# Optimization experiments

Measured on AMD Instinct MI355X. Metric: run time of the kernel, lower is better.

## Reference

```python
import jax, jax.numpy as jnp
import numpy as np
from jax import lax

B, S, H, E, K = 2, 1024, 2048, 16, 4
CAP = int(B * S * 1.5 * K / E)  # capacity = 768
ALPHA = 0.7

def _mlp2(x, w1, b1, w2, b2):
    return jnp.maximum(x @ w1 + b1, 0.0) @ w2 + b2

def setup_inputs() -> dict:
    key = jax.random.key(0)
    ks = iter(jax.random.split(key, 32))
    def w(shape, scale=0.02):
        return (jax.random.normal(next(ks), shape, dtype=jnp.float32) * scale)
    inp = {
        'hidden_states': jax.random.normal(next(ks), (B, S, H), dtype=jnp.float32),
        'mod_image': jax.random.normal(next(ks), (B, S, H), dtype=jnp.float32),
        'mod_genomic': jax.random.normal(next(ks), (B, S, H), dtype=jnp.float32),
        'g_w1': w((H, H)), 'g_b1': jnp.zeros((H,), jnp.float32),
        'g_w2': w((H, E)), 'g_b2': jnp.zeros((E,), jnp.float32),
        'm_w1': w((H, H)), 'm_b1': jnp.zeros((H,), jnp.float32),
        'm_w2': w((H, H)), 'm_b2': jnp.zeros((H,), jnp.float32),
    }
    for p in ('si', 'sg', 'sc', 'sb'):
        inp[p + '_w1'] = w((H, H // 2)); inp[p + '_b1'] = jnp.zeros((H // 2,), jnp.float32)
        inp[p + '_w2'] = w((H // 2, E)); inp[p + '_b2'] = jnp.zeros((E,), jnp.float32)
    return inp

def reference(hidden_states, mod_image, mod_genomic,
              g_w1, g_b1, g_w2, g_b2,
              si_w1, si_b1, si_w2, si_b2,
              sg_w1, sg_b1, sg_w2, sg_b2,
              sc_w1, sc_b1, sc_w2, sc_b2,
              sb_w1, sb_b1, sb_w2, sb_b2,
              m_w1, m_b1, m_w2, m_b2):
    # generalized router probs over experts
    g_probs = jax.nn.softmax(_mlp2(hidden_states, g_w1, g_b1, g_w2, g_b2), axis=-1)
    # missing-modality representation (clinical + biospecimen are missing)
    miss = _mlp2(hidden_states, m_w1, m_b1, m_w2, m_b2)
    # specialized routers: image, genomic (available) + clinical, biospecimen (use miss)
    s_probs = (jax.nn.softmax(_mlp2(mod_image, si_w1, si_b1, si_w2, si_b2), axis=-1)
               + jax.nn.softmax(_mlp2(mod_genomic, sg_w1, sg_b1, sg_w2, sg_b2), axis=-1)
               + jax.nn.softmax(_mlp2(miss, sc_w1, sc_b1, sc_w2, sc_b2), axis=-1)
               + jax.nn.softmax(_mlp2(miss, sb_w1, sb_b1, sb_w2, sb_b2), axis=-1))
    s_probs = s_probs / 2.0  # divided by len(available_modalities) == 2, as in source
    router_probs = ALPHA * g_probs + (1.0 - ALPHA) * s_probs  # [B,S,E]
    top_k_probs, top_k_idx = lax.top_k(router_probs, K)  # [B,S,K]
    top_k_probs = top_k_probs / top_k_probs.sum(axis=-1, keepdims=True)
    onehot = jax.nn.one_hot(top_k_idx, E, dtype=router_probs.dtype)  # [B,S,K,E]
    dmask = onehot.sum(axis=-2)                               # [B,S,E] (0/1: experts distinct)
    cmask = (onehot * top_k_probs[..., None]).sum(axis=-2)    # [B,S,E]
    dispatch = jnp.zeros((B, S, E, CAP), router_probs.dtype).at[..., 0].set(dmask)
    combine = jnp.zeros((B, S, E, CAP), router_probs.dtype).at[..., 0].set(cmask)
    mean_probs = router_probs.mean(axis=(0, 1))  # [E]
    aux_loss = jnp.sum(mean_probs * jnp.log(mean_probs * E + 1e-9))
    return dispatch, combine, router_probs, aux_loss
```

## Files before the change

### kernel.cpp

```cpp
#include <hip/hip_runtime.h>
#include <math.h>
#include <stdint.h>

#define NTOK 2048
#define HDIM 2048
#define HHALF 1024
#define EDIM 16
#define CAPV 768
#define TOPK 4
#define GK 2048

typedef __bf16 bf16x8 __attribute__((ext_vector_type(8)));
typedef __bf16 bf16x4 __attribute__((ext_vector_type(4)));
typedef float f32x4 __attribute__((ext_vector_type(4)));


struct GJobA {
  const __bf16 *Ah, *Al, *Wh, *Wl;
  const float* bias;
  float* Cf; __bf16 *Ch, *Cl;
  int relu, N, blk0;
};
struct GJobsA { GJobA j[6]; };

#define BKA 32
#define NTA 64

#define BARR __builtin_amdgcn_s_barrier()
#define SCHED0 __builtin_amdgcn_sched_barrier(0)
#define PRIO1 __builtin_amdgcn_s_setprio(1)
#define PRIO0 __builtin_amdgcn_s_setprio(0)

__global__ __launch_bounds__(512, 2) void gemm_phased(GJobsA P) {
  __shared__ __align__(16) __bf16 lds[2][4][256 * BKA];

  const int tid = threadIdx.x;
  const int wid = tid >> 6, lane = tid & 63;
  const int lane15 = lane & 15, c0 = lane >> 4;

  const int bid = blockIdx.x;
  int ji = 0;
#pragma unroll
  for (int k = 1; k < 6; ++k)
    if (bid >= P.j[k].blk0) ji = k;
  const GJobA J = P.j[ji];
  const int local = bid - J.blk0;
  const int nbx = J.N >> 8;
  const int bx = local & (nbx - 1);
  const int by = local / nbx;
  const int m0 = by * 256, n0 = bx * 256;

  const int wr = wid >> 2, wc = wid & 3;

  int srow[2], soff[2];
#pragma unroll
  for (int h = 0; h < 2; ++h) {
    int s = tid + h * 512;
    int row = s >> 2;
    srow[h] = row;
    soff[h] = ((s & 3) ^ ((row >> 1) & 3)) * 8;
  }

  int offB[4], offA[2][4];
#pragma unroll
  for (int ni = 0; ni < 4; ++ni) {
    int rb = wc * 64 + ni * 16 + lane15;
    offB[ni] = rb * 64 + ((c0 ^ ((rb >> 1) & 3)) << 4);
  }
#pragma unroll
  for (int mh = 0; mh < 2; ++mh)
#pragma unroll
    for (int i = 0; i < 4; ++i) {
      int ra = wr * 128 + mh * 64 + i * 16 + lane15;
      offA[mh][i] = ra * 64 + ((c0 ^ ((ra >> 1) & 3)) << 4);
    }

#define STAGE2(gptr, grow0, k1, larr)                                          \
  { _Pragma("unroll") for (int h = 0; h < 2; ++h) {                            \
      const __bf16* _src =                                                     \
          (gptr) + (size_t)((grow0) + srow[h]) * GK + (k1) + soff[h];          \
      __builtin_amdgcn_global_load_lds(                                        \
          (const __attribute__((address_space(1))) uint32_t*)_src,             \
          (__attribute__((address_space(3))) uint32_t*)((larr) +               \
              (wid * 64 + h * 512) * 8), 16, 0, 0); } }

#define DSR_A(dst, base, h)                                                    \
  { _Pragma("unroll") for (int i = 0; i < 4; ++i)                              \
      dst[i] = *(const bf16x8*)((base) + offA[h][i]); }
#define DSR_B(dst, base)                                                       \
  { _Pragma("unroll") for (int i = 0; i < 4; ++i)                              \
      dst[i] = *(const bf16x8*)((base) + offB[i]); }
#define MFMA16(af, bf, mh)                                                     \
  { _Pragma("unroll") for (int mi = 0; mi < 4; ++mi)                           \
    _Pragma("unroll") for (int ni = 0; ni < 4; ++ni)                           \
      acc[(mh) * 4 + mi][ni] = __builtin_amdgcn_mfma_f32_16x16x32_bf16(        \
          af[mi], bf[ni], acc[(mh) * 4 + mi][ni], 0, 0, 0); }

  f32x4 acc[8][4];
#pragma unroll
  for (int i = 0; i < 8; ++i)
#pragma unroll
    for (int j = 0; j < 4; ++j) acc[i][j] = (f32x4){0.f, 0.f, 0.f, 0.f};

  STAGE2(J.Ah, m0, 0, lds[0][0]);
  STAGE2(J.Wh, n0, 0, lds[0][2]);
  STAGE2(J.Wl, n0, 0, lds[0][3]);
  STAGE2(J.Al, m0, 0, lds[0][1]);
  asm volatile("s_waitcnt vmcnt(2)" ::: "memory");
  BARR;
  SCHED0;

  bf16x8 ah[4], al[4], bh[4], bl[4];

  for (int t = 0; t < NTA; ++t) {
    const int cur = t & 1, nxt = cur ^ 1;
    const bool hasNext = (t + 1 < NTA);
    const int k1 = (t + 1) * BKA;
    const char* cAh = (const char*)lds[cur][0];
    const char* cAl = (const char*)lds[cur][1];
    const char* cBh = (const char*)lds[cur][2];
    const char* cBl = (const char*)lds[cur][3];

    if (hasNext) {
      STAGE2(J.Ah, m0, k1, lds[nxt][0]);
      STAGE2(J.Wh, n0, k1, lds[nxt][2]);
    }
    DSR_A(ah, cAh, 0);
    DSR_B(bh, cBh);
    DSR_B(bl, cBl);
    PRIO1; MFMA16(ah, bh, 0); PRIO0;
    if (hasNext) { asm volatile("s_waitcnt vmcnt(4)" ::: "memory"); }
    else         { asm volatile("s_waitcnt vmcnt(0)" ::: "memory"); }
    SCHED0;
    BARR;
    SCHED0;
    if (hasNext) {
      STAGE2(J.Wl, n0, k1, lds[nxt][3]);
      STAGE2(J.Al, m0, k1, lds[nxt][1]);
    }
    DSR_A(al, cAl, 0);
    PRIO1; MFMA16(ah, bl, 0); PRIO0;
    DSR_A(ah, cAh, 1);
    PRIO1; MFMA16(al, bh, 0); PRIO0;
    DSR_A(al, cAl, 1);
    PRIO1; MFMA16(ah, bh, 1); PRIO0;
    PRIO1; MFMA16(ah, bl, 1); MFMA16(al, bh, 1); PRIO0;
    if (hasNext) {
      asm volatile("s_waitcnt vmcnt(2)" ::: "memory");
      SCHED0;
      BARR;
      SCHED0;
    }
  }

#pragma unroll
  for (int mh = 0; mh < 2; ++mh)
#pragma unroll
    for (int mi = 0; mi < 4; ++mi)
#pragma unroll
      for (int ni = 0; ni < 4; ++ni) {
        int col = n0 + wc * 64 + ni * 16 + lane15;
        float bv = J.bias[col];
        f32x4 v = acc[mh * 4 + mi][ni];
#pragma unroll
        for (int j = 0; j < 4; ++j) {
          int row = m0 + wr * 128 + mh * 64 + mi * 16 + c0 * 4 + j;
          float x = v[j] + bv;
          if (J.relu) x = fmaxf(x, 0.0f);
          size_t o = (size_t)row * J.N + col;
          if (J.Cf) J.Cf[o] = x;
          if (J.Ch) {
            __bf16 hh = (__bf16)x;
            J.Ch[o] = hh;
            J.Cl[o] = (__bf16)(x - (float)hh);
          }
        }
      }
#undef STAGE2
#undef DSR_A
#undef DSR_B
#undef MFMA16
}

#define BKT 64

struct GJob {
  const __bf16* Ah; const __bf16* Al;
  const __bf16* Wh; const __bf16* Wl;
  const float* bias;
  float* Cf;
  __bf16* Ch; __bf16* Cl;
  int relu; int N; int blk0; int kLen;
};
struct GJobs { GJob j[4]; int njobs; };

__device__ __forceinline__ void stage_tile(const __bf16* __restrict__ g,
                                           int grow0, int k0,
                                           __bf16* lbase, int wid, int lane) {
  int r_in = lane >> 3;
  int swz_elems = ((lane & 7) ^ r_in) << 3;
#pragma unroll
  for (int i = 0; i < 4; ++i) {
    int row0 = wid * 32 + i * 8;
    const __bf16* src = g + (size_t)(grow0 + row0 + r_in) * GK + k0 + swz_elems;
    __builtin_amdgcn_global_load_lds(
        (const __attribute__((address_space(1))) uint32_t*)src,
        (__attribute__((address_space(3))) uint32_t*)(lbase + row0 * BKT),
        16, 0, 0);
  }
}

__global__ __launch_bounds__(256) void gemm_split(GJobs P) {
  __shared__ __align__(16) __bf16 lds[4 * 128 * BKT];
  __bf16* ldsAh = lds;
  __bf16* ldsAl = lds + 8192;
  __bf16* ldsBh = lds + 16384;
  __bf16* ldsBl = lds + 24576;
  const char* cAh = (const char*)ldsAh;
  const char* cAl = (const char*)ldsAl;
  const char* cBh = (const char*)ldsBh;
  const char* cBl = (const char*)ldsBl;

  const int bid = blockIdx.x;
  int ji = 0;
#pragma unroll
  for (int k = 1; k < 4; ++k)
    if (k < P.njobs && bid >= P.j[k].blk0) ji = k;
  const GJob J = P.j[ji];
  const int local = bid - J.blk0;
  const int nbx = J.N >> 7;
  const int bx = local & (nbx - 1);
  const int by = local / nbx;
  const int m0 = by * 128;
  const int n0 = bx * 128;

  const int tid = threadIdx.x;
  const int wid = tid >> 6;
  const int lane = tid & 63;
  const int lane15 = lane & 15;
  const int c0 = lane >> 4;
  const int wr = wid >> 1;
  const int wc = wid & 1;

  int offA[4][2], offB[4][2];
#pragma unroll
  for (int i = 0; i < 4; ++i) {
    int ra = wr * 64 + i * 16 + lane15;
    int rb = wc * 64 + i * 16 + lane15;
#pragma unroll
    for (int ks = 0; ks < 2; ++ks) {
      offA[i][ks] = ra * 128 + (((ks * 4 + c0) ^ (ra & 7)) << 4);
      offB[i][ks] = rb * 128 + (((ks * 4 + c0) ^ (rb & 7)) << 4);
    }
  }

  f32x4 acc[4][4];
#pragma unroll
  for (int i = 0; i < 4; ++i)
#pragma unroll
    for (int j = 0; j < 4; ++j) acc[i][j] = (f32x4){0.f, 0.f, 0.f, 0.f};

  for (int k0 = 0; k0 < J.kLen; k0 += BKT) {
    stage_tile(J.Ah, m0, k0, ldsAh, wid, lane);
    stage_tile(J.Al, m0, k0, ldsAl, wid, lane);
    stage_tile(J.Wh, n0, k0, ldsBh, wid, lane);
    stage_tile(J.Wl, n0, k0, ldsBl, wid, lane);
    __syncthreads();
#pragma unroll
    for (int ks = 0; ks < 2; ++ks) {
      bf16x8 ah[4], al[4], bh[4], bl[4];
#pragma unroll
      for (int i = 0; i < 4; ++i) {
        ah[i] = *(const bf16x8*)(cAh + offA[i][ks]);
        al[i] = *(const bf16x8*)(cAl + offA[i][ks]);
        bh[i] = *(const bf16x8*)(cBh + offB[i][ks]);
        bl[i] = *(const bf16x8*)(cBl + offB[i][ks]);
      }
#pragma unroll
      for (int mi = 0; mi < 4; ++mi)
#pragma unroll
        for (int ni = 0; ni < 4; ++ni) {
          acc[mi][ni] = __builtin_amdgcn_mfma_f32_16x16x32_bf16(
              ah[mi], bh[ni], acc[mi][ni], 0, 0, 0);
          acc[mi][ni] = __builtin_amdgcn_mfma_f32_16x16x32_bf16(
              ah[mi], bl[ni], acc[mi][ni], 0, 0, 0);
          acc[mi][ni] = __builtin_amdgcn_mfma_f32_16x16x32_bf16(
              al[mi], bh[ni], acc[mi][ni], 0, 0, 0);
        }
    }
    __syncthreads();
  }

#pragma unroll
  for (int mi = 0; mi < 4; ++mi) {
#pragma unroll
    for (int ni = 0; ni < 4; ++ni) {
      int col = n0 + wc * 64 + ni * 16 + lane15;
      float bv = J.bias[col];
      f32x4 v = acc[mi][ni];
#pragma unroll
      for (int j = 0; j < 4; ++j) {
        int row = m0 + wr * 64 + mi * 16 + c0 * 4 + j;
        float x = v[j] + bv;
        if (J.relu) x = fmaxf(x, 0.0f);
        size_t o = (size_t)row * J.N + col;
        if (J.Cf) J.Cf[o] = x;
        if (J.Ch) {
          __bf16 hh = (__bf16)x;
          J.Ch[o] = hh;
          J.Cl[o] = (__bf16)(x - (float)hh);
        }
      }
    }
  }
}

struct SJob { const float* in; __bf16* h; __bf16* l; };
struct TJob { const float* W; __bf16* Th; __bf16* Tl; int Nd; };
struct PrepArgs {
  SJob s[4];
  TJob t[6];
  const float* pb2;
  const float* pW1a; const float* pb1a; float* pva;
  const float* pW1b; const float* pb1b; float* pvb;
};

__global__ __launch_bounds__(256) void prep(PrepArgs P) {
  __shared__ float tbuf[32][33];
  const int bid = blockIdx.x;
  const int tid = threadIdx.x;
  if (bid < 16384) {
    SJob J = P.s[bid >> 12];
    int i = (bid & 4095) * 256 + tid;
    float4 v = ((const float4*)J.in)[i];
    bf16x4 hv, lv;
    hv.x = (__bf16)v.x; lv.x = (__bf16)(v.x - (float)hv.x);
    hv.y = (__bf16)v.y; lv.y = (__bf16)(v.y - (float)hv.y);
    hv.z = (__bf16)v.z; lv.z = (__bf16)(v.z - (float)hv.z);
    hv.w = (__bf16)v.w; lv.w = (__bf16)(v.w - (float)hv.w);
    ((bf16x4*)J.h)[i] = hv;
    ((bf16x4*)J.l)[i] = lv;
  } else if (bid < 32768) {
    int local = bid - 16384;
    int ji, ln;
    if (local < 4096)      { ji = 0; ln = local; }
    else if (local < 8192) { ji = 1; ln = local - 4096; }
    else { ji = 2 + ((local - 8192) >> 11); ln = (local - 8192) & 2047; }
    TJob J = P.t[ji];
    int full = (J.Nd == HDIM);
    int n0 = (full ? (ln & 63) : (ln & 31)) * 32;
    int k0 = (full ? (ln >> 6) : (ln >> 5)) * 32;
    int tx = tid & 31, ty = tid >> 5;
#pragma unroll
    for (int i = 0; i < 4; ++i) {
      int kk = ty + i * 8;
      tbuf[kk][tx] = J.W[(size_t)(k0 + kk) * J.Nd + n0 + tx];
    }
    __syncthreads();
#pragma unroll
    for (int i = 0; i < 4; ++i) {
      int nn = ty + i * 8;
      float v = tbuf[tx][nn];
      __bf16 hh = (__bf16)v;
      size_t o = (size_t)(n0 + nn) * GK + k0 + tx;
      J.Th[o] = hh;
      J.Tl[o] = (__bf16)(v - (float)hh);
    }
  } else {
    int local = bid - 32768;
    int side = local >> 5; int r = local & 31;
    const float* W1 = side ? P.pW1b : P.pW1a;
    const float* b1 = side ? P.pb1b : P.pb1a;
    float* v = side ? P.pvb : P.pva;
    int n = (r & 3) * 256 + tid;
    int k0 = (r >> 2) * 256;
    float acc = (k0 == 0) ? b1[n] : 0.0f;
#pragma unroll 8
    for (int k = 0; k < 256; ++k)
      acc = fmaf(P.pb2[k0 + k], W1[(size_t)(k0 + k) * HHALF + n], acc);
    atomicAdd(&v[n], acc);
  }
}

struct LJob { const float* Y; const float* Y2; const float* W2;
              const float* b2; float* L; int K; int relu; };
struct LJobs { LJob j[5]; };
__global__ __launch_bounds__(256) void logits_kernel(LJobs P) {
  const LJob J = P.j[blockIdx.x >> 8];
  const int blk = blockIdx.x & 255;
  const int tid = threadIdx.x;
  const int wid = tid >> 6, lane = tid & 63;
  const int e = lane & 15;
  const int kq = lane >> 4;
  const int tok0 = blk * 8 + wid * 2;
  const float* y0 = J.Y + (size_t)tok0 * J.K;
  const float* y1 = y0 + J.K;
  const float* z0 = J.Y2 + (size_t)tok0 * J.K;
  const float* z1 = z0 + J.K;
  const int KQ = J.K >> 2;
  const int kbase = kq * KQ;
  float a0 = 0.f, a1 = 0.f;
  if (J.relu) {
#pragma unroll 8
    for (int k = 0; k < KQ; ++k) {
      int kk = kbase + k;
      float w = J.W2[(size_t)kk * EDIM + e];
      float v0 = fmaxf(y0[kk] + z0[kk], 0.0f);
      float v1 = fmaxf(y1[kk] + z1[kk], 0.0f);
      a0 = fmaf(v0, w, a0);
      a1 = fmaf(v1, w, a1);
    }
  } else {
#pragma unroll 8
    for (int k = 0; k < KQ; ++k) {
      int kk = kbase + k;
      float w = J.W2[(size_t)kk * EDIM + e];
      a0 = fmaf(y0[kk], w, a0);
      a1 = fmaf(y1[kk], w, a1);
    }
  }
  a0 += __shfl_xor(a0, 16); a0 += __shfl_xor(a0, 32);
  a1 += __shfl_xor(a1, 16); a1 += __shfl_xor(a1, 32);
  if (lane < 16) {
    float b = J.b2[e];
    J.L[(size_t)tok0 * EDIM + e] = a0 + b;
    J.L[(size_t)(tok0 + 1) * EDIM + e] = a1 + b;
  }
}

__device__ __forceinline__ void softmax16(const float* __restrict__ L, float* __restrict__ p) {
  float v[16];
  *(float4*)&v[0]  = *(const float4*)&L[0];
  *(float4*)&v[4]  = *(const float4*)&L[4];
  *(float4*)&v[8]  = *(const float4*)&L[8];
  *(float4*)&v[12] = *(const float4*)&L[12];
  float m = v[0];
#pragma unroll
  for (int e = 1; e < 16; ++e) m = fmaxf(m, v[e]);
  float s = 0.0f;
#pragma unroll
  for (int e = 0; e < 16; ++e) { v[e] = expf(v[e] - m); s += v[e]; }
  float inv = 1.0f / s;
#pragma unroll
  for (int e = 0; e < 16; ++e) p[e] = v[e] * inv;
}

__global__ __launch_bounds__(256) void finalize_kernel(
    const float* __restrict__ Lg, const float* __restrict__ Lsi,
    const float* __restrict__ Lsg, const float* __restrict__ Lsc,
    const float* __restrict__ Lsb,
    float* __restrict__ dispatch, float* __restrict__ combine,
    float* __restrict__ router_probs, float* __restrict__ mean_acc) {
  __shared__ float sm[EDIM];
  int tid = threadIdx.x;
  if (tid < EDIM) sm[tid] = 0.0f;
  __syncthreads();

  int tok = blockIdx.x * 256 + tid;
  float pg[16], ps[16], tmp[16], r[16];
  softmax16(Lg + (size_t)tok * EDIM, pg);
  softmax16(Lsi + (size_t)tok * EDIM, ps);
  softmax16(Lsg + (size_t)tok * EDIM, tmp);
#pragma unroll
  for (int e = 0; e < 16; ++e) ps[e] += tmp[e];
  softmax16(Lsc + (size_t)tok * EDIM, tmp);
#pragma unroll
  for (int e = 0; e < 16; ++e) ps[e] += tmp[e];
  softmax16(Lsb + (size_t)tok * EDIM, tmp);
#pragma unroll
  for (int e = 0; e < 16; ++e) ps[e] += tmp[e];

#pragma unroll
  for (int e = 0; e < 16; ++e) {
    float s = ps[e] * 0.5f;
    r[e] = 0.7f * pg[e] + 0.3f * s;
  }

#pragma unroll
  for (int e = 0; e < 16; e += 4) {
    float4 o = {r[e], r[e + 1], r[e + 2], r[e + 3]};
    *(float4*)&router_probs[(size_t)tok * EDIM + e] = o;
  }

#pragma unroll
  for (int e = 0; e < 16; ++e) atomicAdd(&sm[e], r[e]);

  bool used[16];
#pragma unroll
  for (int e = 0; e < 16; ++e) used[e] = false;
  int idx[TOPK];
  float tp[TOPK];
  float tsum = 0.0f;
#pragma unroll
  for (int j = 0; j < TOPK; ++j) {
    float best = -1.0f;
    int bi = 0;
#pragma unroll
    for (int e = 0; e < 16; ++e) {
      bool take = (!used[e]) && (r[e] > best);
      best = take ? r[e] : best;
      bi = take ? e : bi;
    }
    used[bi] = true;
    idx[j] = bi;
    tp[j] = best;
    tsum += best;
  }
  float invt = 1.0f / tsum;
#pragma unroll
  for (int j = 0; j < TOPK; ++j) {
    size_t off = ((size_t)tok * EDIM + idx[j]) * CAPV;
    dispatch[off] = 1.0f;
    combine[off] = tp[j] * invt;
  }

  __syncthreads();
  if (tid < EDIM) atomicAdd(&mean_acc[tid], sm[tid]);
}

__global__ void aux_kernel(const float* __restrict__ mean_acc, float* __restrict__ out_aux) {
  if (threadIdx.x == 0 && blockIdx.x == 0) {
    float s = 0.0f;
    for (int e = 0; e < EDIM; ++e) {
      float m = mean_acc[e] * (1.0f / (float)NTOK);
      s += m * logf(m * (float)EDIM + 1e-9f);
    }
    *out_aux = s;
  }
}

#define MBYTE (1ull << 20)

extern "C" void kernel_launch(void* const* d_in, const int* in_sizes, int n_in,
                              void* d_out, int out_size, void* d_ws, size_t ws_size,
                              hipStream_t stream) {
  const float* X    = (const float*)d_in[0];
  const float* IMG  = (const float*)d_in[1];
  const float* GEN  = (const float*)d_in[2];
  const float* g_w1 = (const float*)d_in[3];
  const float* g_b1 = (const float*)d_in[4];
  const float* g_w2 = (const float*)d_in[5];
  const float* g_b2 = (const float*)d_in[6];
  const float* m_w1 = (const float*)d_in[7];
  const float* m_b1 = (const float*)d_in[8];
  const float* m_w2 = (const float*)d_in[9];
  const float* m_b2 = (const float*)d_in[10];
  const float* si_w1 = (const float*)d_in[11];
  const float* si_b1 = (const float*)d_in[12];
  const float* si_w2 = (const float*)d_in[13];
  const float* si_b2 = (const float*)d_in[14];
  const float* sg_w1 = (const float*)d_in[15];
  const float* sg_b1 = (const float*)d_in[16];
  const float* sg_w2 = (const float*)d_in[17];
  const float* sg_b2 = (const float*)d_in[18];
  const float* sc_w1 = (const float*)d_in[19];
  const float* sc_b1 = (const float*)d_in[20];
  const float* sc_w2 = (const float*)d_in[21];
  const float* sc_b2 = (const float*)d_in[22];
  const float* sb_w1 = (const float*)d_in[23];
  const float* sb_b1 = (const float*)d_in[24];
  const float* sb_w2 = (const float*)d_in[25];
  const float* sb_b2 = (const float*)d_in[26];

  char* wsb = (char*)d_ws;
  __bf16* Xh    = (__bf16*)(wsb + 0 * MBYTE);
  __bf16* Xl    = (__bf16*)(wsb + 8 * MBYTE);
  __bf16* IMGh  = (__bf16*)(wsb + 16 * MBYTE);
  __bf16* IMGl  = (__bf16*)(wsb + 24 * MBYTE);
  __bf16* GENh  = (__bf16*)(wsb + 32 * MBYTE);
  __bf16* GENl  = (__bf16*)(wsb + 40 * MBYTE);
  __bf16* M2h   = (__bf16*)(wsb + 48 * MBYTE);
  __bf16* M2l   = (__bf16*)(wsb + 56 * MBYTE);
  __bf16* Wm1h  = (__bf16*)(wsb + 64 * MBYTE);
  __bf16* Wm1l  = (__bf16*)(wsb + 72 * MBYTE);
  __bf16* Wg1h  = (__bf16*)(wsb + 80 * MBYTE);
  __bf16* Wg1l  = (__bf16*)(wsb + 88 * MBYTE);
  __bf16* Wsch  = (__bf16*)(wsb + 96 * MBYTE);
  __bf16* Wscl  = (__bf16*)(wsb + 100 * MBYTE);
  __bf16* Wsbh  = (__bf16*)(wsb + 104 * MBYTE);
  __bf16* Wsbl  = (__bf16*)(wsb + 108 * MBYTE);
  __bf16* Wsih  = (__bf16*)(wsb + 112 * MBYTE);
  __bf16* Wsil  = (__bf16*)(wsb + 116 * MBYTE);
  __bf16* Wsgh  = (__bf16*)(wsb + 120 * MBYTE);
  __bf16* Wsgl  = (__bf16*)(wsb + 124 * MBYTE);
  __bf16* H1h   = (__bf16*)(wsb + 128 * MBYTE);
  __bf16* H1l   = (__bf16*)(wsb + 136 * MBYTE);
  __bf16* WPsch = (__bf16*)(wsb + 144 * MBYTE);
  __bf16* WPscl = (__bf16*)(wsb + 148 * MBYTE);
  __bf16* WPsbh = (__bf16*)(wsb + 152 * MBYTE);
  __bf16* WPsbl = (__bf16*)(wsb + 156 * MBYTE);
  float*  YG    = (float*)(wsb + 160 * MBYTE);
  float*  YSI   = (float*)(wsb + 176 * MBYTE);
  float*  YSG   = (float*)(wsb + 184 * MBYTE);
  float*  YSCp0 = (float*)(wsb + 192 * MBYTE);
  float*  YSCp1 = (float*)(wsb + 200 * MBYTE);
  float*  YSBp0 = (float*)(wsb + 208 * MBYTE);
  float*  YSBp1 = (float*)(wsb + 216 * MBYTE);
  float* L0 = (float*)(wsb + 224 * MBYTE);
  float* L1 = L0 + NTOK * EDIM;
  float* L2 = L1 + NTOK * EDIM;
  float* L3 = L2 + NTOK * EDIM;
  float* L4 = L3 + NTOK * EDIM;
  float* meanp = L4 + NTOK * EDIM;
  float* zbias = meanp + EDIM;
  float* vsc = zbias + GK;
  float* vsb = vsc + HHALF;

  float* dispatch = (float*)d_out;
  float* combine = dispatch + (size_t)NTOK * EDIM * CAPV;
  float* rp = combine + (size_t)NTOK * EDIM * CAPV;
  float* aux = rp + (size_t)NTOK * EDIM;

  hipMemsetAsync(d_out, 0, (size_t)out_size * sizeof(float), stream);
  hipMemsetAsync(meanp, 0, (EDIM + GK + 2 * HHALF) * sizeof(float), stream);

  dim3 blk(256);

  {
    PrepArgs p;
    p.s[0] = {X, Xh, Xl};
    p.s[1] = {IMG, IMGh, IMGl};
    p.s[2] = {GEN, GENh, GENl};
    p.s[3] = {m_w2, M2h, M2l};
    p.t[0] = {m_w1, Wm1h, Wm1l, HDIM};
    p.t[1] = {g_w1, Wg1h, Wg1l, HDIM};
    p.t[2] = {sc_w1, Wsch, Wscl, HHALF};
    p.t[3] = {sb_w1, Wsbh, Wsbl, HHALF};
    p.t[4] = {si_w1, Wsih, Wsil, HHALF};
    p.t[5] = {sg_w1, Wsgh, Wsgl, HHALF};
    p.pb2 = m_b2;
    p.pW1a = sc_w1; p.pb1a = sc_b1; p.pva = vsc;
    p.pW1b = sb_w1; p.pb1b = sb_b1; p.pvb = vsb;
    prep<<<32832, blk, 0, stream>>>(p);
  }

  {
    GJobsA g;
    g.j[0] = {Xh, Xl, Wm1h, Wm1l, m_b1, nullptr, H1h, H1l, 1, HDIM, 0};
    g.j[1] = {Xh, Xl, Wg1h, Wg1l, g_b1, YG, nullptr, nullptr, 1, HDIM, 64};
    g.j[2] = {IMGh, IMGl, Wsih, Wsil, si_b1, YSI, nullptr, nullptr, 1, HHALF, 128};
    g.j[3] = {GENh, GENl, Wsgh, Wsgl, sg_b1, YSG, nullptr, nullptr, 1, HHALF, 160};
    g.j[4] = {Wsch, Wscl, M2h, M2l, zbias, nullptr, WPsch, WPscl, 0, HDIM, 192};
    g.j[5] = {Wsbh, Wsbl, M2h, M2l, zbias, nullptr, WPsbh, WPsbl, 0, HDIM, 224};
    gemm_phased<<<256, dim3(512), 0, stream>>>(g);
  }

  {
    GJobs g;
    g.j[0] = {H1h, H1l, WPsch, WPscl, vsc, YSCp0, nullptr, nullptr, 0, HHALF, 0, 1024};
    g.j[1] = {H1h + 1024, H1l + 1024, WPsch + 1024, WPscl + 1024, zbias, YSCp1,
              nullptr, nullptr, 0, HHALF, 128, 1024};
    g.j[2] = {H1h, H1l, WPsbh, WPsbl, vsb, YSBp0, nullptr, nullptr, 0, HHALF, 256, 1024};
    g.j[3] = {H1h + 1024, H1l + 1024, WPsbh + 1024, WPsbl + 1024, zbias, YSBp1,
              nullptr, nullptr, 0, HHALF, 384, 1024};
    g.njobs = 4;
    gemm_split<<<512, blk, 0, stream>>>(g);
  }

  {
    LJobs l;
    l.j[0] = {YG, YG, g_w2, g_b2, L0, HDIM, 0};
    l.j[1] = {YSI, YSI, si_w2, si_b2, L1, HHALF, 0};
    l.j[2] = {YSG, YSG, sg_w2, sg_b2, L2, HHALF, 0};
    l.j[3] = {YSCp0, YSCp1, sc_w2, sc_b2, L3, HHALF, 1};
    l.j[4] = {YSBp0, YSBp1, sb_w2, sb_b2, L4, HHALF, 1};
    logits_kernel<<<5 * 256, blk, 0, stream>>>(l);
  }

  finalize_kernel<<<NTOK / 256, blk, 0, stream>>>(L0, L1, L2, L3, L4,
                                                  dispatch, combine, rp, meanp);
  aux_kernel<<<1, 64, 0, stream>>>(meanp, aux);
}
```

Before: 397.6 us.

## Fold output zeroing into prep and overlap independent logits with split GEMM

Drops the separate hipMemsetAsync over the large dispatch/combine output and has extra blocks of the prep kernel zero it. The three logits jobs that depend only on earlier GEMM outputs move into the split-GEMM launch as extra blocks so they run alongside it, and the remaining logits kernel now handles only the two split-K jobs. The GEMM epilogue loses its unused relu and bf16-split branches. This cuts launches and lets bandwidth-bound work share the GPU with compute-bound tiles, at the cost of larger LDS-sized blocks being launched for simple logits work.

```diff
diff --git a/kernel.cpp b/kernel.cpp
--- a/kernel.cpp
+++ b/kernel.cpp
@@ -189,29 +189,46 @@
   const __bf16* Wh; const __bf16* Wl;
   const float* bias;
   float* Cf;
-  __bf16* Ch; __bf16* Cl;
-  int relu; int N; int blk0; int kLen;
+  int N; int blk0; int kLen;
 };
-struct GJobs { GJob j[4]; int njobs; };
-
-__device__ __forceinline__ void stage_tile(const __bf16* __restrict__ g,
-                                           int grow0, int k0,
-                                           __bf16* lbase, int wid, int lane) {
-  int r_in = lane >> 3;
-  int swz_elems = ((lane & 7) ^ r_in) << 3;
-#pragma unroll
-  for (int i = 0; i < 4; ++i) {
-    int row0 = wid * 32 + i * 8;
-    const __bf16* src = g + (size_t)(grow0 + row0 + r_in) * GK + k0 + swz_elems;
-    __builtin_amdgcn_global_load_lds(
-        (const __attribute__((address_space(1))) uint32_t*)src,
-        (__attribute__((address_space(3))) uint32_t*)(lbase + row0 * BKT),
-        16, 0, 0);
-  }
-}
-
-__global__ __launch_bounds__(256) void gemm_split(GJobs P) {
+struct LJob3 { const float* Y; const float* W2; const float* b2; float* L; int K; };
+struct StageBArgs { GJob gj[4]; LJob3 lj[3]; };
+
+__global__ __launch_bounds__(256) void stageB(StageBArgs P) {
   __shared__ __align__(16) __bf16 lds[4 * 128 * BKT];
+  const int bid = blockIdx.x;
+  const int tid = threadIdx.x;
+
+  if (bid >= 512) {
+    const int lid = bid - 512;
+    const LJob3 J = P.lj[lid >> 8];
+    const int blk = lid & 255;
+    const int wid = tid >> 6, lane = tid & 63;
+    const int e = lane & 15;
+    const int kq = lane >> 4;
+    const int tok0 = blk * 8 + wid * 2;
+    const float* y0 = J.Y + (size_t)tok0 * J.K;
+    const float* y1 = y0 + J.K;
+    const int KQ = J.K >> 2;
+    const int kbase = kq * KQ;
+    float a0 = 0.f, a1 = 0.f;
+#pragma unroll 8
+    for (int k = 0; k < KQ; ++k) {
+      int kk = kbase + k;
+      float w = J.W2[(size_t)kk * EDIM + e];
+      a0 = fmaf(y0[kk], w, a0);
+      a1 = fmaf(y1[kk], w, a1);
+    }
+    a0 += __shfl_xor(a0, 16); a0 += __shfl_xor(a0, 32);
+    a1 += __shfl_xor(a1, 16); a1 += __shfl_xor(a1, 32);
+    if (lane < 16) {
+      float b = J.b2[e];
+      J.L[(size_t)tok0 * EDIM + e] = a0 + b;
+      J.L[(size_t)(tok0 + 1) * EDIM + e] = a1 + b;
+    }
+    return;
+  }
+
   __bf16* ldsAh = lds;
   __bf16* ldsAl = lds + 8192;
   __bf16* ldsBh = lds + 16384;
@@ -221,12 +238,11 @@
   const char* cBh = (const char*)ldsBh;
   const char* cBl = (const char*)ldsBl;
 
-  const int bid = blockIdx.x;
   int ji = 0;
 #pragma unroll
   for (int k = 1; k < 4; ++k)
-    if (k < P.njobs && bid >= P.j[k].blk0) ji = k;
-  const GJob J = P.j[ji];
+    if (bid >= P.gj[k].blk0) ji = k;
+  const GJob J = P.gj[ji];
   const int local = bid - J.blk0;
   const int nbx = J.N >> 7;
   const int bx = local & (nbx - 1);
@@ -234,7 +250,6 @@
   const int m0 = by * 128;
   const int n0 = bx * 128;
 
-  const int tid = threadIdx.x;
   const int wid = tid >> 6;
   const int lane = tid & 63;
   const int lane15 = lane & 15;
@@ -260,11 +275,23 @@
 #pragma unroll
     for (int j = 0; j < 4; ++j) acc[i][j] = (f32x4){0.f, 0.f, 0.f, 0.f};
 
+  const int r_in = lane >> 3;
+  const int swz_elems = ((lane & 7) ^ r_in) << 3;
+#define STG(gptr, grow0, k0, lbase)                                            \
+  { _Pragma("unroll") for (int i = 0; i < 4; ++i) {                            \
+      int row0 = wid * 32 + i * 8;                                             \
+      const __bf16* src =                                                      \
+          (gptr) + (size_t)((grow0) + row0 + r_in) * GK + (k0) + swz_elems;    \
+      __builtin_amdgcn_global_load_lds(                                        \
+          (const __attribute__((address_space(1))) uint32_t*)src,              \
+          (__attribute__((address_space(3))) uint32_t*)((lbase) + row0 * BKT), \
+          16, 0, 0); } }
+
   for (int k0 = 0; k0 < J.kLen; k0 += BKT) {
-    stage_tile(J.Ah, m0, k0, ldsAh, wid, lane);
-    stage_tile(J.Al, m0, k0, ldsAl, wid, lane);
-    stage_tile(J.Wh, n0, k0, ldsBh, wid, lane);
-    stage_tile(J.Wl, n0, k0, ldsBl, wid, lane);
+    STG(J.Ah, m0, k0, ldsAh);
+    STG(J.Al, m0, k0, ldsAl);
+    STG(J.Wh, n0, k0, ldsBh);
+    STG(J.Wl, n0, k0, ldsBl);
     __syncthreads();
 #pragma unroll
     for (int ks = 0; ks < 2; ++ks) {
@@ -290,6 +317,7 @@
     }
     __syncthreads();
   }
+#undef STG
 
 #pragma unroll
   for (int mi = 0; mi < 4; ++mi) {
@@ -302,14 +330,7 @@
       for (int j = 0; j < 4; ++j) {
         int row = m0 + wr * 64 + mi * 16 + c0 * 4 + j;
         float x = v[j] + bv;
-        if (J.relu) x = fmaxf(x, 0.0f);
-        size_t o = (size_t)row * J.N + col;
-        if (J.Cf) J.Cf[o] = x;
-        if (J.Ch) {
-          __bf16 hh = (__bf16)x;
-          J.Ch[o] = hh;
-          J.Cl[o] = (__bf16)(x - (float)hh);
-        }
+        J.Cf[(size_t)row * J.N + col] = x;
       }
     }
   }
@@ -318,6 +339,7 @@
 struct SJob { const float* in; __bf16* h; __bf16* l; };
 struct TJob { const float* W; __bf16* Th; __bf16* Tl; int Nd; };
 struct PrepArgs {
+  float* dout; int out_size; int zb;
   SJob s[4];
   TJob t[6];
   const float* pb2;
@@ -329,9 +351,24 @@
   __shared__ float tbuf[32][33];
   const int bid = blockIdx.x;
   const int tid = threadIdx.x;
-  if (bid < 16384) {
-    SJob J = P.s[bid >> 12];
-    int i = (bid & 4095) * 256 + tid;
+  if (bid < P.zb) {
+    const int n4 = P.out_size >> 2;
+    float4 z = {0.f, 0.f, 0.f, 0.f};
+#pragma unroll
+    for (int it = 0; it < 4; ++it) {
+      int i = bid * 1024 + it * 256 + tid;
+      if (i < n4) ((float4*)P.dout)[i] = z;
+    }
+    if (bid == 0 && tid < 4) {
+      int i = (n4 << 2) + tid;
+      if (i < P.out_size) P.dout[i] = 0.0f;
+    }
+    return;
+  }
+  const int rb = bid - P.zb;
+  if (rb < 16384) {
+    SJob J = P.s[rb >> 12];
+    int i = (rb & 4095) * 256 + tid;
     float4 v = ((const float4*)J.in)[i];
     bf16x4 hv, lv;
     hv.x = (__bf16)v.x; lv.x = (__bf16)(v.x - (float)hv.x);
@@ -340,8 +377,8 @@
     hv.w = (__bf16)v.w; lv.w = (__bf16)(v.w - (float)hv.w);
     ((bf16x4*)J.h)[i] = hv;
     ((bf16x4*)J.l)[i] = lv;
-  } else if (bid < 32768) {
-    int local = bid - 16384;
+  } else if (rb < 32768) {
+    int local = rb - 16384;
     int ji, ln;
     if (local < 4096)      { ji = 0; ln = local; }
     else if (local < 8192) { ji = 1; ln = local - 4096; }
@@ -367,7 +404,7 @@
       J.Tl[o] = (__bf16)(v - (float)hh);
     }
   } else {
-    int local = bid - 32768;
+    int local = rb - 32768;
     int side = local >> 5; int r = local & 31;
     const float* W1 = side ? P.pW1b : P.pW1a;
     const float* b1 = side ? P.pb1b : P.pb1a;
@@ -383,8 +420,8 @@
 }
 
 struct LJob { const float* Y; const float* Y2; const float* W2;
-              const float* b2; float* L; int K; int relu; };
-struct LJobs { LJob j[5]; };
+              const float* b2; float* L; };
+struct LJobs { LJob j[2]; };
 __global__ __launch_bounds__(256) void logits_kernel(LJobs P) {
   const LJob J = P.j[blockIdx.x >> 8];
   const int blk = blockIdx.x & 255;
@@ -393,31 +430,21 @@
   const int e = lane & 15;
   const int kq = lane >> 4;
   const int tok0 = blk * 8 + wid * 2;
-  const float* y0 = J.Y + (size_t)tok0 * J.K;
-  const float* y1 = y0 + J.K;
-  const float* z0 = J.Y2 + (size_t)tok0 * J.K;
-  const float* z1 = z0 + J.K;
-  const int KQ = J.K >> 2;
+  const float* y0 = J.Y + (size_t)tok0 * HHALF;
+  const float* y1 = y0 + HHALF;
+  const float* z0 = J.Y2 + (size_t)tok0 * HHALF;
+  const float* z1 = z0 + HHALF;
+  const int KQ = HHALF >> 2;
   const int kbase = kq * KQ;
   float a0 = 0.f, a1 = 0.f;
-  if (J.relu) {
 #pragma unroll 8
-    for (int k = 0; k < KQ; ++k) {
-      int kk = kbase + k;
-      float w = J.W2[(size_t)kk * EDIM + e];
-      float v0 = fmaxf(y0[kk] + z0[kk], 0.0f);
-      float v1 = fmaxf(y1[kk] + z1[kk], 0.0f);
-      a0 = fmaf(v0, w, a0);
-      a1 = fmaf(v1, w, a1);
-    }
-  } else {
-#pragma unroll 8
-    for (int k = 0; k < KQ; ++k) {
-      int kk = kbase + k;
-      float w = J.W2[(size_t)kk * EDIM + e];
-      a0 = fmaf(y0[kk], w, a0);
-      a1 = fmaf(y1[kk], w, a1);
-    }
+  for (int k = 0; k < KQ; ++k) {
+    int kk = kbase + k;
+    float w = J.W2[(size_t)kk * EDIM + e];
+    float v0 = fmaxf(y0[kk] + z0[kk], 0.0f);
+    float v1 = fmaxf(y1[kk] + z1[kk], 0.0f);
+    a0 = fmaf(v0, w, a0);
+    a1 = fmaf(v1, w, a1);
   }
   a0 += __shfl_xor(a0, 16); a0 += __shfl_xor(a0, 32);
   a1 += __shfl_xor(a1, 16); a1 += __shfl_xor(a1, 32);
@@ -611,13 +638,14 @@
   float* rp = combine + (size_t)NTOK * EDIM * CAPV;
   float* aux = rp + (size_t)NTOK * EDIM;
 
-  hipMemsetAsync(d_out, 0, (size_t)out_size * sizeof(float), stream);
   hipMemsetAsync(meanp, 0, (EDIM + GK + 2 * HHALF) * sizeof(float), stream);
 
   dim3 blk(256);
+  const int zb = (out_size + 4095) / 4096;
 
   {
     PrepArgs p;
+    p.dout = (float*)d_out; p.out_size = out_size; p.zb = zb;
     p.s[0] = {X, Xh, Xl};
     p.s[1] = {IMG, IMGh, IMGl};
     p.s[2] = {GEN, GENh, GENl};
@@ -631,7 +659,7 @@
     p.pb2 = m_b2;
     p.pW1a = sc_w1; p.pb1a = sc_b1; p.pva = vsc;
     p.pW1b = sb_w1; p.pb1b = sb_b1; p.pvb = vsb;
-    prep<<<32832, blk, 0, stream>>>(p);
+    prep<<<zb + 32832, blk, 0, stream>>>(p);
   }
 
   {
@@ -646,25 +674,24 @@
   }
 
   {
-    GJobs g;
-    g.j[0] = {H1h, H1l, WPsch, WPscl, vsc, YSCp0, nullptr, nullptr, 0, HHALF, 0, 1024};
-    g.j[1] = {H1h + 1024, H1l + 1024, WPsch + 1024, WPscl + 1024, zbias, YSCp1,
-              nullptr, nullptr, 0, HHALF, 128, 1024};
-    g.j[2] = {H1h, H1l, WPsbh, WPsbl, vsb, YSBp0, nullptr, nullptr, 0, HHALF, 256, 1024};
-    g.j[3] = {H1h + 1024, H1l + 1024, WPsbh + 1024, WPsbl + 1024, zbias, YSBp1,
-              nullptr, nullptr, 0, HHALF, 384, 1024};
-    g.njobs = 4;
-    gemm_split<<<512, blk, 0, stream>>>(g);
+    StageBArgs s;
+    s.gj[0] = {H1h, H1l, WPsch, WPscl, vsc, YSCp0, HHALF, 0, 1024};
+    s.gj[1] = {H1h + 1024, H1l + 1024, WPsch + 1024, WPscl + 1024, zbias, YSCp1,
+               HHALF, 128, 1024};
+    s.gj[2] = {H1h, H1l, WPsbh, WPsbl, vsb, YSBp0, HHALF, 256, 1024};
+    s.gj[3] = {H1h + 1024, H1l + 1024, WPsbh + 1024, WPsbl + 1024, zbias, YSBp1,
+               HHALF, 384, 1024};
+    s.lj[0] = {YG, g_w2, g_b2, L0, HDIM};
+    s.lj[1] = {YSI, si_w2, si_b2, L1, HHALF};
+    s.lj[2] = {YSG, sg_w2, sg_b2, L2, HHALF};
+    stageB<<<512 + 768, blk, 0, stream>>>(s);
   }
 
   {
     LJobs l;
-    l.j[0] = {YG, YG, g_w2, g_b2, L0, HDIM, 0};
-    l.j[1] = {YSI, YSI, si_w2, si_b2, L1, HHALF, 0};
-    l.j[2] = {YSG, YSG, sg_w2, sg_b2, L2, HHALF, 0};
-    l.j[3] = {YSCp0, YSCp1, sc_w2, sc_b2, L3, HHALF, 1};
-    l.j[4] = {YSBp0, YSBp1, sb_w2, sb_b2, L4, HHALF, 1};
-    logits_kernel<<<5 * 256, blk, 0, stream>>>(l);
+    l.j[0] = {YSCp0, YSCp1, sc_w2, sc_b2, L3};
+    l.j[1] = {YSBp0, YSBp1, sb_w2, sb_b2, L4};
+    logits_kernel<<<2 * 256, blk, 0, stream>>>(l);
   }
 
   finalize_kernel<<<NTOK / 256, blk, 0, stream>>>(L0, L1, L2, L3, L4,
```

Result: no change. 405.0 us (+1.9%).
